# Performance work log

Measured on AMD Instinct MI355X. Metric: run time of the kernel, lower is better.

The kernel has to match this reference:

```python
import jax, jax.numpy as jnp
import numpy as np
from jax import lax

C = 256
B, T = 4, 4
AH, AW = 32, 32
VH, VW = 56, 56
EPS = 1e-5


def _pool_matrix(n_in, n_out):
    # PyTorch adaptive_avg_pool1d semantics per axis
    M = np.zeros((n_out, n_in), np.float32)
    for i in range(n_out):
        s = (i * n_in) // n_out
        e = -((-(i + 1) * n_in) // n_out)  # ceil
        M[i, s:e] = 1.0 / (e - s)
    return jnp.asarray(M)


def _bilinear_matrix(n_in, n_out):
    # PyTorch bilinear, align_corners=False
    scale = n_in / n_out
    M = np.zeros((n_out, n_in), np.float32)
    for i in range(n_out):
        src = (i + 0.5) * scale - 0.5
        src = min(max(src, 0.0), n_in - 1)
        i0 = int(np.floor(src))
        i1 = min(i0 + 1, n_in - 1)
        w1 = src - i0
        M[i, i0] += 1.0 - w1
        M[i, i1] += w1
    return jnp.asarray(M)


def _group_norm1(x, w, b):
    # GroupNorm(1, C): normalize over (C,H,W) per sample, per-channel affine
    mu = jnp.mean(x, axis=(1, 2, 3), keepdims=True)
    var = jnp.mean(jnp.square(x - mu), axis=(1, 2, 3), keepdims=True)
    xn = (x - mu) * lax.rsqrt(var + EPS)
    return xn * w[None, :, None, None] + b[None, :, None, None]


def _dwconv(x, w, pad, dil):
    c = x.shape[1]
    return lax.conv_general_dilated(
        x, w, window_strides=(1, 1), padding=[(pad, pad), (pad, pad)],
        rhs_dilation=(dil, dil), feature_group_count=c,
        dimension_numbers=('NCHW', 'OIHW', 'NCHW'))


def _pwconv(x, w, b):
    return jnp.einsum('oc,bchw->bohw', w, x) + b[None, :, None, None]


def _lkm(x, gn_w, gn_b, dw7, dw3, pw_w, pw_b):
    x = _group_norm1(x, gn_w, gn_b)
    x = _dwconv(x, dw7, pad=3, dil=1) + _dwconv(x, dw3, pad=3, dil=3)
    x = _pwconv(x, pw_w, pw_b)
    return jax.nn.gelu(x, approximate=False)


def setup_inputs() -> dict:
    key = jax.random.key(0)
    ks = jax.random.split(key, 20)
    s = lambda k, shape, scale=0.05: jax.random.normal(k, shape, jnp.float32) * scale
    return {
        'a': jax.random.normal(ks[0], (B, C, AH, AW), jnp.float32),
        'v': jax.random.normal(ks[1], (B * T, C, VH, VW), jnp.float32),
        'a_gn_w': jnp.ones((C,), jnp.float32), 'a_gn_b': jnp.zeros((C,), jnp.float32),
        'a_dw7': s(ks[2], (C, 1, 7, 7)), 'a_dw3': s(ks[3], (C, 1, 3, 3)),
        'a_pw_w': s(ks[4], (C, C)), 'a_pw_b': jnp.zeros((C,), jnp.float32),
        'v_gn_w': jnp.ones((C,), jnp.float32), 'v_gn_b': jnp.zeros((C,), jnp.float32),
        'v_dw7': s(ks[5], (C, 1, 7, 7)), 'v_dw3': s(ks[6], (C, 1, 3, 3)),
        'v_pw_w': s(ks[7], (C, C)), 'v_pw_b': jnp.zeros((C,), jnp.float32),
        'gate_a_w': s(ks[8], (C, C)), 'gate_a_b': jnp.zeros((C,), jnp.float32),
        'gate_v_w': s(ks[9], (C, C)), 'gate_v_b': jnp.zeros((C,), jnp.float32),
        'scale_a': jnp.ones((1,), jnp.float32), 'scale_v': jnp.ones((1,), jnp.float32),
    }


def reference(a, v, a_gn_w, a_gn_b, a_dw7, a_dw3, a_pw_w, a_pw_b,
              v_gn_w, v_gn_b, v_dw7, v_dw3, v_pw_w, v_pw_b,
              gate_a_w, gate_a_b, gate_v_w, gate_v_b, scale_a, scale_v):
    strength_a = strength_v = 1.0
    temp = 1.0
    b = a.shape[0]
    vb, c, vh, vw = v.shape
    t = vb // b
    ah, aw = a.shape[2], a.shape[3]

    a_feat = _lkm(a, a_gn_w, a_gn_b, a_dw7, a_dw3, a_pw_w, a_pw_b)
    v_feat = _lkm(v, v_gn_w, v_gn_b, v_dw7, v_dw3, v_pw_w, v_pw_b)

    v_feat_mean = v_feat.reshape(b, t, c, vh, vw).mean(axis=1) if t > 1 else v_feat

    if (vh, vw) != (ah, aw):
        Ph, Pw = _pool_matrix(vh, ah), _pool_matrix(vw, aw)
        v_for_a = jnp.einsum('oh,bchw,pw->bcop', Ph, v_feat_mean, Pw)
    else:
        v_for_a = v_feat_mean
    gate_a = jax.nn.sigmoid(_pwconv(v_for_a, gate_a_w, gate_a_b) / temp)

    if (ah, aw) != (vh, vw):
        Rh, Rw = _bilinear_matrix(ah, vh), _bilinear_matrix(aw, vw)
        a_for_v = jnp.einsum('oh,bchw,pw->bcop', Rh, a_feat, Rw)
    else:
        a_for_v = a_feat
    gate_v = jax.nn.sigmoid(_pwconv(a_for_v, gate_v_w, gate_v_b) / temp)
    if t > 1:
        gate_v = jnp.broadcast_to(gate_v[:, None], (b, t, c, vh, vw)).reshape(vb, c, vh, vw)

    a_out = a + strength_a * (scale_a[0] * (a_feat * gate_a))
    v_out = v + strength_v * (scale_v[0] * (v_feat * gate_v))
    return (a_out, v_out)
```

## Files before the change

kernel.cpp:

```cpp
#include <hip/hip_runtime.h>
#include <math.h>

#define C_   256
#define B_   4
#define T_   4
#define AH_  32
#define AW_  32
#define VH_  56
#define VW_  56
#define AHW  (AH_*AW_)
#define VHW  (VH_*VW_)
#define NA_  (B_*C_*AHW)
#define NV_  (B_*T_*C_*VHW)
#define NAV_ (B_*C_*VHW)

typedef unsigned short u16;
typedef short s16x8 __attribute__((ext_vector_type(8)));
typedef unsigned short u16x8 __attribute__((ext_vector_type(8)));
typedef unsigned short u16x4 __attribute__((ext_vector_type(4)));
typedef float f32x4 __attribute__((ext_vector_type(4)));

__device__ __forceinline__ u16 f2b(float f) {
  unsigned u = __float_as_uint(f);
  u += 0x7FFFu + ((u >> 16) & 1u);
  return (u16)(u >> 16);
}
__device__ __forceinline__ float b2f(u16 h) {
  return __uint_as_float((unsigned)h << 16);
}
__device__ __forceinline__ float gelu_f(float x) {
  float x2 = x * x;
  float e = __expf(x * (-1.5957691216f - 0.0713548162f * x2));
  return x * __builtin_amdgcn_rcpf(1.f + e);
}
__device__ __forceinline__ float sigmoid_f(float x) {
  return __builtin_amdgcn_rcpf(1.f + __expf(-x));
}

__global__ __launch_bounds__(256) void cvt_bf16_4(
    const float* __restrict__ s0, const float* __restrict__ s1,
    const float* __restrict__ s2, const float* __restrict__ s3,
    u16* __restrict__ dst)
{
  int g = blockIdx.x >> 5;
  const float* src = (g == 0) ? s0 : (g == 1) ? s1 : (g == 2) ? s2 : s3;
  size_t i = ((size_t)(blockIdx.x & 31) * 256 + threadIdx.x) * 8;
  float4 v0 = *(const float4*)(src + i);
  float4 v1 = *(const float4*)(src + i + 4);
  u16x8 o = {f2b(v0.x), f2b(v0.y), f2b(v0.z), f2b(v0.w),
             f2b(v1.x), f2b(v1.y), f2b(v1.z), f2b(v1.w)};
  *(u16x8*)(dst + (size_t)g * 65536 + i) = o;
}

__global__ __launch_bounds__(256) void gn_reduce1m(
    const float* __restrict__ a, const float* __restrict__ v,
    float* __restrict__ part)
{
  int samp = blockIdx.y, chunk = blockIdx.x;
  const float* x; int per;
  if (samp < 4) { x = a + (size_t)samp * (C_ * AHW); per = (C_ * AHW / 4) / 128; }
  else          { x = v + (size_t)(samp - 4) * (C_ * VHW); per = (C_ * VHW / 4) / 128; }
  const float4* xb = (const float4*)x + (size_t)chunk * per;
  float s = 0.f, s2 = 0.f;
  for (int i = threadIdx.x; i < per; i += 256) {
    float4 q = xb[i];
    s  += q.x + q.y + q.z + q.w;
    s2 += q.x*q.x + q.y*q.y + q.z*q.z + q.w*q.w;
  }
  __shared__ float sh1[256], sh2[256];
  sh1[threadIdx.x] = s; sh2[threadIdx.x] = s2;
  __syncthreads();
  for (int st = 128; st > 0; st >>= 1) {
    if (threadIdx.x < st) {
      sh1[threadIdx.x] += sh1[threadIdx.x + st];
      sh2[threadIdx.x] += sh2[threadIdx.x + st];
    }
    __syncthreads();
  }
  if (threadIdx.x == 0) {
    part[(samp * 128 + chunk) * 2 + 0] = sh1[0];
    part[(samp * 128 + chunk) * 2 + 1] = sh2[0];
  }
}

__global__ __launch_bounds__(128) void gn_reduce2m(
    const float* __restrict__ part, float* __restrict__ stats)
{
  int samp = blockIdx.x;
  int t = threadIdx.x;
  __shared__ float sh1[128], sh2[128];
  sh1[t] = part[(samp * 128 + t) * 2 + 0];
  sh2[t] = part[(samp * 128 + t) * 2 + 1];
  __syncthreads();
  for (int st = 64; st > 0; st >>= 1) {
    if (t < st) { sh1[t] += sh1[t + st]; sh2[t] += sh2[t + st]; }
    __syncthreads();
  }
  if (t == 0) {
    float invN = (samp < 4) ? 1.f / (float)(C_ * AHW) : 1.f / (float)(C_ * VHW);
    float mu  = sh1[0] * invN;
    float var = sh2[0] * invN - mu * mu;
    stats[samp * 2 + 0] = mu;
    stats[samp * 2 + 1] = rsqrtf(var + 1e-5f);
  }
}

__global__ __launch_bounds__(256) void gn_dwconv_all(
    const float* __restrict__ xa, const float* __restrict__ xv,
    const float* __restrict__ stats,
    const float* __restrict__ a_gn_w, const float* __restrict__ a_gn_b,
    const float* __restrict__ a_dw7, const float* __restrict__ a_dw3,
    const float* __restrict__ v_gn_w, const float* __restrict__ v_gn_b,
    const float* __restrict__ v_dw7, const float* __restrict__ v_dw3,
    u16* __restrict__ outa, u16* __restrict__ outv)
{
  __shared__ float tile[62 * 64];
  __shared__ float comb[49];
  const int t = threadIdx.x;
  if (blockIdx.x < 1024) {
    constexpr int TH = 38, TW = 38, TWP = 44;
    const int nc = blockIdx.x;
    const int n = nc >> 8, c = nc & 255;
    const float mu = stats[2 * n], rstd = stats[2 * n + 1];
    const float gsc = a_gn_w[c] * rstd;
    const float gsh = a_gn_b[c] - mu * gsc;
    if (t < 49) comb[t] = a_dw7[c * 49 + t];
    __syncthreads();
    if (t < 9) comb[(t / 3) * 21 + (t % 3) * 3] += a_dw3[c * 9 + t];
    const float* xc = xa + (size_t)nc * AHW;
    for (int idx = t; idx < TH * TW; idx += 256) {
      int th = idx / TW, tw = idx - th * TW;
      int h = th - 3, w = tw - 3;
      float val = 0.f;
      if (h >= 0 && h < 32 && w >= 0 && w < 32) val = xc[h * 32 + w] * gsc + gsh;
      tile[th * TWP + tw] = val;
    }
    __syncthreads();
    if (t < 128) {
      const int rg = t >> 3, cq = t & 7;
      const int r0 = rg * 2, w0 = cq * 4;
      float acc[2][4];
      #pragma unroll
      for (int r = 0; r < 2; ++r)
        #pragma unroll
        for (int j = 0; j < 4; ++j) acc[r][j] = 0.f;
      #pragma unroll
      for (int i = 0; i < 8; ++i) {
        const float* row = &tile[(r0 + i) * TWP + w0];
        float4 ra = *(const float4*)(row);
        float4 rb = *(const float4*)(row + 4);
        float2 rc = *(const float2*)(row + 8);
        float rr[10] = {ra.x, ra.y, ra.z, ra.w, rb.x, rb.y, rb.z, rb.w, rc.x, rc.y};
        #pragma unroll
        for (int ky = 0; ky < 7; ++ky) {
          int orow = i - ky;
          if (orow >= 0 && orow < 2) {
            #pragma unroll
            for (int kx = 0; kx < 7; ++kx) {
              float wg = comb[ky * 7 + kx];
              #pragma unroll
              for (int j = 0; j < 4; ++j)
                acc[orow][j] = fmaf(rr[kx + j], wg, acc[orow][j]);
            }
          }
        }
      }
      u16* oc = outa + (size_t)nc * AHW;
      #pragma unroll
      for (int r = 0; r < 2; ++r) {
        u16x4 res = {f2b(acc[r][0]), f2b(acc[r][1]), f2b(acc[r][2]), f2b(acc[r][3])};
        *(u16x4*)&oc[(r0 + r) * 32 + w0] = res;
      }
    }
  } else {
    const int nc = blockIdx.x - 1024;
    const int n = nc >> 8, c = nc & 255;
    const float mu = stats[8 + 2 * n], rstd = stats[8 + 2 * n + 1];
    const float gsc = v_gn_w[c] * rstd;
    const float gsh = v_gn_b[c] - mu * gsc;
    if (t < 49) comb[t] = v_dw7[c * 49 + t];
    __syncthreads();
    if (t < 9) comb[(t / 3) * 21 + (t % 3) * 3] += v_dw3[c * 9 + t];
    const float* xc = xv + (size_t)nc * VHW;
    if (t < 208) {
      int row, q;
      if (t < 96) { int ri = t >> 4; row = (ri < 3) ? ri : ri + 56; q = t & 15; }
      else        { int r = t - 96; row = 3 + (r >> 1); q = (r & 1) ? 15 : 0; }
      int qz = q ^ (row & 7);
      f32x4 z = {0.f, 0.f, 0.f, 0.f};
      *(f32x4*)&tile[row * 64 + qz * 4] = z;
    }
    #pragma unroll
    for (int it = 0; it < 4; ++it) {
      int idx = t + it * 256;
      if (idx < 784) {
        int row = idx / 14, q = idx - row * 14;
        float4 v = *(const float4*)(xc + row * VW_ + q * 4);
        int trow = row + 3;
        int tq = (q + 1) ^ (trow & 7);
        f32x4 sv = {v.x * gsc + gsh, v.y * gsc + gsh,
                    v.z * gsc + gsh, v.w * gsc + gsh};
        *(f32x4*)&tile[trow * 64 + tq * 4] = sv;
      }
    }
    __syncthreads();
    if (t < 196) {
      const int rg = t / 14, cq = t - rg * 14;
      const int r0 = rg * 4;
      float acc[4][4];
      #pragma unroll
      for (int r = 0; r < 4; ++r)
        #pragma unroll
        for (int j = 0; j < 4; ++j) acc[r][j] = 0.f;
      #pragma unroll
      for (int i = 0; i < 10; ++i) {
        int trow = r0 + i;
        const float* rowb = &tile[trow * 64];
        int rz = trow & 7;
        float rr[12];
        #pragma unroll
        for (int k = 0; k < 3; ++k) {
          int qk = (cq + k) ^ rz;
          f32x4 rv = *(const f32x4*)(rowb + qk * 4);
          rr[4 * k + 0] = rv[0]; rr[4 * k + 1] = rv[1];
          rr[4 * k + 2] = rv[2]; rr[4 * k + 3] = rv[3];
        }
        #pragma unroll
        for (int ky = 0; ky < 7; ++ky) {
          int orow = i - ky;
          if (orow >= 0 && orow < 4) {
            #pragma unroll
            for (int kx = 0; kx < 7; ++kx) {
              float wg = comb[ky * 7 + kx];
              #pragma unroll
              for (int j = 0; j < 4; ++j)
                acc[orow][j] = fmaf(rr[j + kx + 1], wg, acc[orow][j]);
            }
          }
        }
      }
      u16* oc = outv + (size_t)nc * VHW;
      #pragma unroll
      for (int r = 0; r < 4; ++r) {
        u16x4 res = {f2b(acc[r][0]), f2b(acc[r][1]), f2b(acc[r][2]), f2b(acc[r][3])};
        *(u16x4*)&oc[(r0 + r) * VW_ + cq * 4] = res;
      }
    }
  }
}

__global__ __launch_bounds__(256) void transpose_all(
    const u16* __restrict__ ina, u16* __restrict__ outa,
    const u16* __restrict__ inv, u16* __restrict__ outv)
{
  __shared__ u16 tile[64 * 68];
  const int t = threadIdx.x;
  int bid = blockIdx.x;
  const u16* in; u16* outp; int HW, PT;
  if (bid < 256) { in = ina; outp = outa; HW = AHW; PT = 16; }
  else           { bid -= 256; in = inv; outp = outv; HW = VHW; PT = 49; }
  int px = bid % PT; int rem = bid / PT;
  int cy = rem & 3, s = rem >> 2;
  const int p0 = px * 64, c0 = cy * 64;
  const u16* src = in + ((size_t)s * 256 + c0) * HW + p0;
  #pragma unroll
  for (int it = 0; it < 2; ++it) {
    int slot = it * 256 + t;
    int cr = slot >> 3, ch = slot & 7;
    u16x8 v = *(const u16x8*)(src + (size_t)cr * HW + ch * 8);
    u16x4 lo = {v[0], v[1], v[2], v[3]}, hi = {v[4], v[5], v[6], v[7]};
    *(u16x4*)&tile[cr * 68 + ch * 8] = lo;
    *(u16x4*)&tile[cr * 68 + ch * 8 + 4] = hi;
  }
  __syncthreads();
  int pr = t >> 2, ch = t & 3;
  u16* dst = outp + ((size_t)s * HW + p0 + pr) * 256 + c0;
  #pragma unroll
  for (int jj = 0; jj < 2; ++jj) {
    int cb = ch * 8 + jj * 32;
    u16x8 o;
    #pragma unroll
    for (int j = 0; j < 8; ++j) o[j] = tile[(cb + j) * 68 + pr];
    *(u16x8*)(dst + cb) = o;
  }
}

template<int ACT, int WPC, int WCP, int NBA, int PTA, int PTV>
__global__ __launch_bounds__(256) void mfma_pw2(
    const u16* __restrict__ Xa, const u16* __restrict__ Wa,
    const float* __restrict__ ba, u16* __restrict__ outa_pc, u16* __restrict__ outa_cp,
    const u16* __restrict__ Xv, const u16* __restrict__ Wv,
    const float* __restrict__ bv, u16* __restrict__ outv_pc, u16* __restrict__ outv_cp)
{
  __shared__ __align__(16) char smem[(256 * 72 + 64 * 72) * 2];
  u16* Wl = (u16*)smem;
  u16* Xl = (u16*)smem + 256 * 72;
  float* Tt = (float*)smem;
  u16*  Pc = (u16*)smem;
  const int t = threadIdx.x;
  const int lane = t & 63, wid = t >> 6;
  const int g = lane >> 4, lr = lane & 15;
  int bid = blockIdx.x;
  const u16 *X, *W; const float* bias; u16 *out_pc, *out_cp; int HW, px, s;
  if (bid < NBA) {
    X = Xa; W = Wa; bias = ba; out_pc = outa_pc; out_cp = outa_cp;
    HW = PTA * 64; px = bid % PTA; s = bid / PTA;
  } else {
    bid -= NBA;
    X = Xv; W = Wv; bias = bv; out_pc = outv_pc; out_cp = outv_cp;
    HW = PTV * 64; px = bid % PTV; s = bid / PTV;
  }
  const int p0 = px * 64;
  const u16* Xs = X + ((size_t)s * HW + p0) * 256;
  f32x4 acc[4][4] = {};
  u16x8 stw[8], stx[2];
  #pragma unroll
  for (int it = 0; it < 8; ++it) {
    int slot = it * 256 + t, row = slot >> 3, ch = slot & 7;
    stw[it] = *(const u16x8*)(W + row * 256 + ch * 8);
  }
  #pragma unroll
  for (int it = 0; it < 2; ++it) {
    int slot = it * 256 + t, row = slot >> 3, ch = slot & 7;
    stx[it] = *(const u16x8*)(Xs + (size_t)row * 256 + ch * 8);
  }
  for (int kt = 0; kt < 4; ++kt) {
    __syncthreads();
    #pragma unroll
    for (int it = 0; it < 8; ++it) {
      int slot = it * 256 + t, row = slot >> 3, ch = slot & 7;
      *(u16x8*)&Wl[row * 72 + ch * 8] = stw[it];
    }
    #pragma unroll
    for (int it = 0; it < 2; ++it) {
      int slot = it * 256 + t, row = slot >> 3, ch = slot & 7;
      *(u16x8*)&Xl[row * 72 + ch * 8] = stx[it];
    }
    __syncthreads();
    if (kt < 3) {
      const int k1 = (kt + 1) * 64;
      #pragma unroll
      for (int it = 0; it < 8; ++it) {
        int slot = it * 256 + t, row = slot >> 3, ch = slot & 7;
        stw[it] = *(const u16x8*)(W + row * 256 + k1 + ch * 8);
      }
      #pragma unroll
      for (int it = 0; it < 2; ++it) {
        int slot = it * 256 + t, row = slot >> 3, ch = slot & 7;
        stx[it] = *(const u16x8*)(Xs + (size_t)row * 256 + k1 + ch * 8);
      }
    }
    #pragma unroll
    for (int ks = 0; ks < 2; ++ks) {
      s16x8 af[4], bf[4];
      #pragma unroll
      for (int m = 0; m < 4; ++m) {
        int row = wid * 64 + m * 16 + lr;
        af[m] = *(const s16x8*)&Wl[row * 72 + ks * 32 + g * 8];
      }
      #pragma unroll
      for (int n = 0; n < 4; ++n) {
        int row = n * 16 + lr;
        bf[n] = *(const s16x8*)&Xl[row * 72 + ks * 32 + g * 8];
      }
      #pragma unroll
      for (int m = 0; m < 4; ++m)
        #pragma unroll
        for (int n = 0; n < 4; ++n)
          acc[m][n] = __builtin_amdgcn_mfma_f32_16x16x32_bf16(af[m], bf[n], acc[m][n], 0, 0, 0);
    }
  }
  __syncthreads();
  #pragma unroll
  for (int m = 0; m < 4; ++m) {
    int ob = wid * 64 + m * 16 + g * 4;
    float4 b4 = *(const float4*)&bias[ob];
    float bb[4] = {b4.x, b4.y, b4.z, b4.w};
    #pragma unroll
    for (int n = 0; n < 4; ++n)
      #pragma unroll
      for (int r = 0; r < 4; ++r) {
        float y = acc[m][n][r] + bb[r];
        acc[m][n][r] = (ACT == 0) ? gelu_f(y) : sigmoid_f(y);
      }
  }
  if (WPC) {
    #pragma unroll
    for (int m = 0; m < 4; ++m) {
      int obase = wid * 64 + m * 16 + g * 4;
      #pragma unroll
      for (int n = 0; n < 4; ++n) {
        int p = n * 16 + lr;
        int op = obase ^ ((p & 7) << 3);
        u16x4 pk = {f2b(acc[m][n][0]), f2b(acc[m][n][1]), f2b(acc[m][n][2]), f2b(acc[m][n][3])};
        *(u16x4*)&Pc[p * 256 + op] = pk;
      }
    }
    __syncthreads();
    int pr = t >> 2;
    u16* dst = out_pc + ((size_t)s * HW + p0 + pr) * 256;
    #pragma unroll
    for (int j = 0; j < 8; ++j) {
      int o = (j * 4 + (t & 3)) * 8;
      int op = o ^ ((pr & 7) << 3);
      u16x8 vv = *(const u16x8*)&Pc[pr * 256 + op];
      *(u16x8*)(dst + o) = vv;
    }
  }
  if (WCP) {
    #pragma unroll
    for (int ho = 0; ho < 2; ++ho) {
      __syncthreads();
      if ((wid >> 1) == ho) {
        #pragma unroll
        for (int m = 0; m < 4; ++m) {
          int ol = (wid & 1) * 64 + m * 16 + g * 4;
          #pragma unroll
          for (int n = 0; n < 4; ++n) {
            int p = n * 16 + lr, q = p >> 2;
            #pragma unroll
            for (int r = 0; r < 4; ++r) {
              int orow = ol + r;
              Tt[orow * 64 + ((q ^ (orow & 15)) << 2) + (p & 3)] = acc[m][n][r];
            }
          }
        }
      }
      __syncthreads();
      #pragma unroll
      for (int it = 0; it < 8; ++it) {
        int slot = it * 256 + t;
        int ol = slot >> 4, q = slot & 15;
        float4 v4 = *(const float4*)&Tt[ol * 64 + ((q ^ (ol & 15)) << 2)];
        u16x4 pk = {f2b(v4.x), f2b(v4.y), f2b(v4.z), f2b(v4.w)};
        int o = ho * 128 + ol;
        *(u16x4*)(out_cp + ((size_t)s * 256 + o) * HW + p0 + q * 4) = pk;
      }
    }
  }
}

__global__ __launch_bounds__(256) void pool_bilin(
    const u16* __restrict__ vf, u16* __restrict__ vfa,
    const u16* __restrict__ af, u16* __restrict__ afv)
{
  int c = threadIdx.x;
  int pb = blockIdx.x;
  if (pb < 4096) {
    int ow = pb & 31, oh = (pb >> 5) & 31, b = pb >> 10;
    int sh = (oh * VH_) >> 5, eh = ((oh + 1) * VH_ + 31) >> 5;
    int sw = (ow * VW_) >> 5, ew = ((ow + 1) * VW_ + 31) >> 5;
    float acc = 0.f;
    for (int tt = 0; tt < T_; ++tt)
      for (int ih = sh; ih < eh; ++ih)
        for (int iw = sw; iw < ew; ++iw)
          acc += b2f(vf[((size_t)(b * T_ + tt) * VHW + ih * VW_ + iw) * 256 + c]);
    vfa[(size_t)pb * 256 + c] = f2b(acc / (float)(T_ * (eh - sh) * (ew - sw)));
  } else {
    pb -= 4096;
    int ow = pb % VW_; int tmp = pb / VW_; int oh = tmp % VH_; int b = tmp / VH_;
    const float sc = (float)AH_ / (float)VH_;
    float srh = fminf(fmaxf((oh + 0.5f) * sc - 0.5f, 0.f), (float)(AH_ - 1));
    float srw = fminf(fmaxf((ow + 0.5f) * sc - 0.5f, 0.f), (float)(AW_ - 1));
    int h0 = (int)srh, w0 = (int)srw;
    int h1 = min(h0 + 1, AH_ - 1), w1 = min(w0 + 1, AW_ - 1);
    float fh = srh - (float)h0, fw = srw - (float)w0;
    const u16* base = af + (size_t)b * AHW * 256 + c;
    float v00 = b2f(base[(h0 * AW_ + w0) * 256]), v01 = b2f(base[(h0 * AW_ + w1) * 256]);
    float v10 = b2f(base[(h1 * AW_ + w0) * 256]), v11 = b2f(base[(h1 * AW_ + w1) * 256]);
    float top = v00 + (v01 - v00) * fw;
    float bot = v10 + (v11 - v10) * fw;
    afv[(size_t)pb * 256 + c] = f2b(top + (bot - top) * fh);
  }
}

__global__ __launch_bounds__(256) void final_av(
    const float* __restrict__ a, const u16* __restrict__ afcp,
    const u16* __restrict__ gacp, const float* __restrict__ sa,
    const float* __restrict__ v, const u16* __restrict__ vfcp,
    const u16* __restrict__ gvcp, const float* __restrict__ sv,
    float* __restrict__ out)
{
  int bid = blockIdx.x;
  if (bid < 512) {
    size_t i = ((size_t)bid * 256 + threadIdx.x) * 8;
    float s = sa[0];
    float4 a0 = *(const float4*)(a + i), a1 = *(const float4*)(a + i + 4);
    u16x8 f = *(const u16x8*)(afcp + i);
    u16x8 gg = *(const u16x8*)(gacp + i);
    float4 o0 = {a0.x + s * b2f(f[0]) * b2f(gg[0]), a0.y + s * b2f(f[1]) * b2f(gg[1]),
                 a0.z + s * b2f(f[2]) * b2f(gg[2]), a0.w + s * b2f(f[3]) * b2f(gg[3])};
    float4 o1 = {a1.x + s * b2f(f[4]) * b2f(gg[4]), a1.y + s * b2f(f[5]) * b2f(gg[5]),
                 a1.z + s * b2f(f[6]) * b2f(gg[6]), a1.w + s * b2f(f[7]) * b2f(gg[7])};
    *(float4*)(out + i) = o0;
    *(float4*)(out + i + 4) = o1;
  } else {
    size_t i = ((size_t)(bid - 512) * 256 + threadIdx.x) * 8;
    const size_t PER = (size_t)C_ * VHW;
    int bt = (int)(i / PER);
    size_t rem = i - (size_t)bt * PER;
    const u16* gp = gvcp + (size_t)(bt >> 2) * PER + rem;
    float s = sv[0];
    float4 v0 = *(const float4*)(v + i), v1 = *(const float4*)(v + i + 4);
    u16x8 f = *(const u16x8*)(vfcp + i);
    u16x8 gg = *(const u16x8*)gp;
    float4 o0 = {v0.x + s * b2f(f[0]) * b2f(gg[0]), v0.y + s * b2f(f[1]) * b2f(gg[1]),
                 v0.z + s * b2f(f[2]) * b2f(gg[2]), v0.w + s * b2f(f[3]) * b2f(gg[3])};
    float4 o1 = {v1.x + s * b2f(f[4]) * b2f(gg[4]), v1.y + s * b2f(f[5]) * b2f(gg[5]),
                 v1.z + s * b2f(f[6]) * b2f(gg[6]), v1.w + s * b2f(f[7]) * b2f(gg[7])};
    float* ov = out + NA_;
    *(float4*)(ov + i) = o0;
    *(float4*)(ov + i + 4) = o1;
  }
}

extern "C" void kernel_launch(void* const* d_in, const int* in_sizes, int n_in,
                              void* d_out, int out_size, void* d_ws, size_t ws_size,
                              hipStream_t stream)
{
  const float* a        = (const float*)d_in[0];
  const float* v        = (const float*)d_in[1];
  const float* a_gn_w   = (const float*)d_in[2];
  const float* a_gn_b   = (const float*)d_in[3];
  const float* a_dw7    = (const float*)d_in[4];
  const float* a_dw3    = (const float*)d_in[5];
  const float* a_pw_w   = (const float*)d_in[6];
  const float* a_pw_b   = (const float*)d_in[7];
  const float* v_gn_w   = (const float*)d_in[8];
  const float* v_gn_b   = (const float*)d_in[9];
  const float* v_dw7    = (const float*)d_in[10];
  const float* v_dw3    = (const float*)d_in[11];
  const float* v_pw_w   = (const float*)d_in[12];
  const float* v_pw_b   = (const float*)d_in[13];
  const float* gate_a_w = (const float*)d_in[14];
  const float* gate_a_b = (const float*)d_in[15];
  const float* gate_v_w = (const float*)d_in[16];
  const float* gate_v_b = (const float*)d_in[17];
  const float* scale_a  = (const float*)d_in[18];
  const float* scale_v  = (const float*)d_in[19];
  float* out = (float*)d_out;
  char* wsb = (char*)d_ws;

  const size_t SZ_V  = (size_t)NV_ * 2;
  const size_t SZ_AV = (size_t)NAV_ * 2;
  const size_t SZ_A  = (size_t)NA_ * 2;
  u16* dwv_b    = (u16*)(wsb + 0);
  u16* vfeat_cp = (u16*)(wsb + 0);
  u16* dwvT     = (u16*)(wsb + SZ_V);
  u16* afv      = (u16*)(wsb + SZ_V);
  u16* gatev_cp = (u16*)(wsb + SZ_V + SZ_AV);
  u16* vfeat_pc = (u16*)(wsb + 2 * SZ_V);
  u16* dwa_b    = (u16*)(wsb + 3 * SZ_V);
  u16* dwaT     = (u16*)(wsb + 3 * SZ_V + SZ_A);
  u16* afeat_pc = (u16*)(wsb + 3 * SZ_V + 2 * SZ_A);
  u16* afeat_cp = (u16*)(wsb + 3 * SZ_V + 3 * SZ_A);
  u16* vfa      = (u16*)(wsb + 3 * SZ_V + 4 * SZ_A);
  u16* gatea_cp = (u16*)(wsb + 3 * SZ_V + 5 * SZ_A);
  u16* w_bf     = (u16*)(wsb + 3 * SZ_V + 6 * SZ_A);
  float* pf     = (float*)(wsb + 3 * SZ_V + 6 * SZ_A + 4 * 65536 * 2);
  float* part   = pf;
  float* stats  = pf + 5120;
  u16* wA = w_bf, *wV = w_bf + 65536, *wGA = w_bf + 131072, *wGV = w_bf + 196608;

  cvt_bf16_4<<<128, 256, 0, stream>>>(a_pw_w, v_pw_w, gate_a_w, gate_v_w, w_bf);

  gn_reduce1m<<<dim3(128, 20), 256, 0, stream>>>(a, v, part);
  gn_reduce2m<<<20, 128, 0, stream>>>(part, stats);

  gn_dwconv_all<<<5120, 256, 0, stream>>>(a, v, stats,
      a_gn_w, a_gn_b, a_dw7, a_dw3, v_gn_w, v_gn_b, v_dw7, v_dw3, dwa_b, dwv_b);

  transpose_all<<<3392, 256, 0, stream>>>(dwa_b, dwaT, dwv_b, dwvT);

  mfma_pw2<0, 1, 1, 64, 16, 49><<<848, 256, 0, stream>>>(
      dwaT, wA, a_pw_b, afeat_pc, afeat_cp,
      dwvT, wV, v_pw_b, vfeat_pc, vfeat_cp);

  pool_bilin<<<16640, 256, 0, stream>>>(vfeat_pc, vfa, afeat_pc, afv);

  mfma_pw2<1, 0, 1, 64, 16, 49><<<260, 256, 0, stream>>>(
      vfa, wGA, gate_a_b, nullptr, gatea_cp,
      afv, wGV, gate_v_b, nullptr, gatev_cp);

  final_av<<<6784, 256, 0, stream>>>(a, afeat_cp, gatea_cp, scale_a,
                                     v, vfeat_cp, gatev_cp, scale_v, out);
}
```

Before: 148.0 us.

## Read channel-major activations directly in pointwise GEMM, drop transpose and pc outputs

The pointwise MFMA kernel now loads channel-major (NCHW) activations and transposes them into LDS itself, so the separate transpose kernel is gone. It also stops writing the pixel-major copy of the features, and pool/bilinear is rewritten to work on channel-major data, one block per (batch, channel). This removes a full read and write of the large v intermediates plus one launch. In exchange the GEMM's global loads become narrower strided 8-byte reads, and the pooling access pattern changes.

```diff
diff --git a/kernel.cpp b/kernel.cpp
--- a/kernel.cpp
+++ b/kernel.cpp
@@ -249,81 +249,44 @@
   }
 }
 
-__global__ __launch_bounds__(256) void transpose_all(
-    const u16* __restrict__ ina, u16* __restrict__ outa,
-    const u16* __restrict__ inv, u16* __restrict__ outv)
-{
-  __shared__ u16 tile[64 * 68];
-  const int t = threadIdx.x;
-  int bid = blockIdx.x;
-  const u16* in; u16* outp; int HW, PT;
-  if (bid < 256) { in = ina; outp = outa; HW = AHW; PT = 16; }
-  else           { bid -= 256; in = inv; outp = outv; HW = VHW; PT = 49; }
-  int px = bid % PT; int rem = bid / PT;
-  int cy = rem & 3, s = rem >> 2;
-  const int p0 = px * 64, c0 = cy * 64;
-  const u16* src = in + ((size_t)s * 256 + c0) * HW + p0;
-  #pragma unroll
-  for (int it = 0; it < 2; ++it) {
-    int slot = it * 256 + t;
-    int cr = slot >> 3, ch = slot & 7;
-    u16x8 v = *(const u16x8*)(src + (size_t)cr * HW + ch * 8);
-    u16x4 lo = {v[0], v[1], v[2], v[3]}, hi = {v[4], v[5], v[6], v[7]};
-    *(u16x4*)&tile[cr * 68 + ch * 8] = lo;
-    *(u16x4*)&tile[cr * 68 + ch * 8 + 4] = hi;
-  }
-  __syncthreads();
-  int pr = t >> 2, ch = t & 3;
-  u16* dst = outp + ((size_t)s * HW + p0 + pr) * 256 + c0;
-  #pragma unroll
-  for (int jj = 0; jj < 2; ++jj) {
-    int cb = ch * 8 + jj * 32;
-    u16x8 o;
-    #pragma unroll
-    for (int j = 0; j < 8; ++j) o[j] = tile[(cb + j) * 68 + pr];
-    *(u16x8*)(dst + cb) = o;
-  }
-}
-
-template<int ACT, int WPC, int WCP, int NBA, int PTA, int PTV>
+template<int ACT, int NBA, int PTA, int PTV>
 __global__ __launch_bounds__(256) void mfma_pw2(
     const u16* __restrict__ Xa, const u16* __restrict__ Wa,
-    const float* __restrict__ ba, u16* __restrict__ outa_pc, u16* __restrict__ outa_cp,
+    const float* __restrict__ ba, u16* __restrict__ outa_cp,
     const u16* __restrict__ Xv, const u16* __restrict__ Wv,
-    const float* __restrict__ bv, u16* __restrict__ outv_pc, u16* __restrict__ outv_cp)
-{
-  __shared__ __align__(16) char smem[(256 * 72 + 64 * 72) * 2];
+    const float* __restrict__ bv, u16* __restrict__ outv_cp)
+{
+  __shared__ __align__(16) char smem[256 * 72 * 2 + 64 * 68 * 2];
   u16* Wl = (u16*)smem;
   u16* Xl = (u16*)smem + 256 * 72;
   float* Tt = (float*)smem;
-  u16*  Pc = (u16*)smem;
   const int t = threadIdx.x;
   const int lane = t & 63, wid = t >> 6;
   const int g = lane >> 4, lr = lane & 15;
   int bid = blockIdx.x;
-  const u16 *X, *W; const float* bias; u16 *out_pc, *out_cp; int HW, px, s;
+  const u16 *X, *W; const float* bias; u16* out_cp; int HW, px, s;
   if (bid < NBA) {
-    X = Xa; W = Wa; bias = ba; out_pc = outa_pc; out_cp = outa_cp;
+    X = Xa; W = Wa; bias = ba; out_cp = outa_cp;
     HW = PTA * 64; px = bid % PTA; s = bid / PTA;
   } else {
     bid -= NBA;
-    X = Xv; W = Wv; bias = bv; out_pc = outv_pc; out_cp = outv_cp;
+    X = Xv; W = Wv; bias = bv; out_cp = outv_cp;
     HW = PTV * 64; px = bid % PTV; s = bid / PTV;
   }
   const int p0 = px * 64;
-  const u16* Xs = X + ((size_t)s * HW + p0) * 256;
+  const u16* Xs = X + (size_t)s * 256 * HW + p0;
+  const int cg = t >> 4, pg = t & 15;
   f32x4 acc[4][4] = {};
-  u16x8 stw[8], stx[2];
+  u16x8 stw[8];
+  u16x4 stc[4];
   #pragma unroll
   for (int it = 0; it < 8; ++it) {
     int slot = it * 256 + t, row = slot >> 3, ch = slot & 7;
     stw[it] = *(const u16x8*)(W + row * 256 + ch * 8);
   }
   #pragma unroll
-  for (int it = 0; it < 2; ++it) {
-    int slot = it * 256 + t, row = slot >> 3, ch = slot & 7;
-    stx[it] = *(const u16x8*)(Xs + (size_t)row * 256 + ch * 8);
-  }
+  for (int cc = 0; cc < 4; ++cc)
+    stc[cc] = *(const u16x4*)(Xs + (size_t)(cg * 4 + cc) * HW + pg * 4);
   for (int kt = 0; kt < 4; ++kt) {
     __syncthreads();
     #pragma unroll
@@ -332,9 +295,9 @@
       *(u16x8*)&Wl[row * 72 + ch * 8] = stw[it];
     }
     #pragma unroll
-    for (int it = 0; it < 2; ++it) {
-      int slot = it * 256 + t, row = slot >> 3, ch = slot & 7;
-      *(u16x8*)&Xl[row * 72 + ch * 8] = stx[it];
+    for (int pp = 0; pp < 4; ++pp) {
+      u16x4 vv = {stc[0][pp], stc[1][pp], stc[2][pp], stc[3][pp]};
+      *(u16x4*)&Xl[(pg * 4 + pp) * 68 + cg * 4] = vv;
     }
     __syncthreads();
     if (kt < 3) {
@@ -345,10 +308,8 @@
         stw[it] = *(const u16x8*)(W + row * 256 + k1 + ch * 8);
       }
       #pragma unroll
-      for (int it = 0; it < 2; ++it) {
-        int slot = it * 256 + t, row = slot >> 3, ch = slot & 7;
-        stx[it] = *(const u16x8*)(Xs + (size_t)row * 256 + k1 + ch * 8);
-      }
+      for (int cc = 0; cc < 4; ++cc)
+        stc[cc] = *(const u16x4*)(Xs + (size_t)(k1 + cg * 4 + cc) * HW + pg * 4);
     }
     #pragma unroll
     for (int ks = 0; ks < 2; ++ks) {
@@ -361,7 +322,7 @@
       #pragma unroll
       for (int n = 0; n < 4; ++n) {
         int row = n * 16 + lr;
-        bf[n] = *(const s16x8*)&Xl[row * 72 + ks * 32 + g * 8];
+        bf[n] = *(const s16x8*)&Xl[row * 68 + ks * 32 + g * 8];
       }
       #pragma unroll
       for (int m = 0; m < 4; ++m)
@@ -384,93 +345,83 @@
         acc[m][n][r] = (ACT == 0) ? gelu_f(y) : sigmoid_f(y);
       }
   }
-  if (WPC) {
-    #pragma unroll
-    for (int m = 0; m < 4; ++m) {
-      int obase = wid * 64 + m * 16 + g * 4;
-      #pragma unroll
-      for (int n = 0; n < 4; ++n) {
-        int p = n * 16 + lr;
-        int op = obase ^ ((p & 7) << 3);
-        u16x4 pk = {f2b(acc[m][n][0]), f2b(acc[m][n][1]), f2b(acc[m][n][2]), f2b(acc[m][n][3])};
-        *(u16x4*)&Pc[p * 256 + op] = pk;
-      }
-    }
-    __syncthreads();
-    int pr = t >> 2;
-    u16* dst = out_pc + ((size_t)s * HW + p0 + pr) * 256;
-    #pragma unroll
-    for (int j = 0; j < 8; ++j) {
-      int o = (j * 4 + (t & 3)) * 8;
-      int op = o ^ ((pr & 7) << 3);
-      u16x8 vv = *(const u16x8*)&Pc[pr * 256 + op];
-      *(u16x8*)(dst + o) = vv;
-    }
-  }
-  if (WCP) {
-    #pragma unroll
-    for (int ho = 0; ho < 2; ++ho) {
-      __syncthreads();
-      if ((wid >> 1) == ho) {
-        #pragma unroll
-        for (int m = 0; m < 4; ++m) {
-          int ol = (wid & 1) * 64 + m * 16 + g * 4;
+  #pragma unroll
+  for (int ho = 0; ho < 2; ++ho) {
+    __syncthreads();
+    if ((wid >> 1) == ho) {
+      #pragma unroll
+      for (int m = 0; m < 4; ++m) {
+        int ol = (wid & 1) * 64 + m * 16 + g * 4;
+        #pragma unroll
+        for (int n = 0; n < 4; ++n) {
+          int p = n * 16 + lr, q = p >> 2;
           #pragma unroll
-          for (int n = 0; n < 4; ++n) {
-            int p = n * 16 + lr, q = p >> 2;
-            #pragma unroll
-            for (int r = 0; r < 4; ++r) {
-              int orow = ol + r;
-              Tt[orow * 64 + ((q ^ (orow & 15)) << 2) + (p & 3)] = acc[m][n][r];
-            }
+          for (int r = 0; r < 4; ++r) {
+            int orow = ol + r;
+            Tt[orow * 64 + ((q ^ (orow & 15)) << 2) + (p & 3)] = acc[m][n][r];
           }
         }
       }
-      __syncthreads();
-      #pragma unroll
-      for (int it = 0; it < 8; ++it) {
-        int slot = it * 256 + t;
-        int ol = slot >> 4, q = slot & 15;
-        float4 v4 = *(const float4*)&Tt[ol * 64 + ((q ^ (ol & 15)) << 2)];
-        u16x4 pk = {f2b(v4.x), f2b(v4.y), f2b(v4.z), f2b(v4.w)};
-        int o = ho * 128 + ol;
-        *(u16x4*)(out_cp + ((size_t)s * 256 + o) * HW + p0 + q * 4) = pk;
-      }
-    }
-  }
-}
-
-__global__ __launch_bounds__(256) void pool_bilin(
-    const u16* __restrict__ vf, u16* __restrict__ vfa,
-    const u16* __restrict__ af, u16* __restrict__ afv)
-{
-  int c = threadIdx.x;
-  int pb = blockIdx.x;
-  if (pb < 4096) {
-    int ow = pb & 31, oh = (pb >> 5) & 31, b = pb >> 10;
-    int sh = (oh * VH_) >> 5, eh = ((oh + 1) * VH_ + 31) >> 5;
-    int sw = (ow * VW_) >> 5, ew = ((ow + 1) * VW_ + 31) >> 5;
-    float acc = 0.f;
-    for (int tt = 0; tt < T_; ++tt)
-      for (int ih = sh; ih < eh; ++ih)
-        for (int iw = sw; iw < ew; ++iw)
-          acc += b2f(vf[((size_t)(b * T_ + tt) * VHW + ih * VW_ + iw) * 256 + c]);
-    vfa[(size_t)pb * 256 + c] = f2b(acc / (float)(T_ * (eh - sh) * (ew - sw)));
+    }
+    __syncthreads();
+    #pragma unroll
+    for (int it = 0; it < 8; ++it) {
+      int slot = it * 256 + t;
+      int ol = slot >> 4, q = slot & 15;
+      float4 v4 = *(const float4*)&Tt[ol * 64 + ((q ^ (ol & 15)) << 2)];
+      u16x4 pk = {f2b(v4.x), f2b(v4.y), f2b(v4.z), f2b(v4.w)};
+      int o = ho * 128 + ol;
+      *(u16x4*)(out_cp + ((size_t)s * 256 + o) * HW + p0 + q * 4) = pk;
+    }
+  }
+}
+
+__global__ __launch_bounds__(256) void pool_bilin_cp(
+    const u16* __restrict__ vf_cp, u16* __restrict__ vfa_cp,
+    const u16* __restrict__ af_cp, u16* __restrict__ afv_cp)
+{
+  const int t = threadIdx.x;
+  int bid = blockIdx.x;
+  if (bid < 1024) {
+    int b = bid >> 8, c = bid & 255;
+    u16* dst = vfa_cp + ((size_t)(b * 256 + c) << 10);
+    #pragma unroll
+    for (int k = 0; k < 4; ++k) {
+      int idx = t + k * 256;
+      int oh = idx >> 5, ow = idx & 31;
+      int sh = (oh * VH_) >> 5, eh = ((oh + 1) * VH_ + 31) >> 5;
+      int sw = (ow * VW_) >> 5, ew = ((ow + 1) * VW_ + 31) >> 5;
+      float acc = 0.f;
+      for (int tt = 0; tt < T_; ++tt) {
+        const u16* base = vf_cp + ((size_t)((b * T_ + tt) * 256 + c)) * VHW;
+        for (int ih = sh; ih < eh; ++ih)
+          for (int iw = sw; iw < ew; ++iw)
+            acc += b2f(base[ih * VW_ + iw]);
+      }
+      dst[idx] = f2b(acc / (float)(T_ * (eh - sh) * (ew - sw)));
+    }
   } else {
-    pb -= 4096;
-    int ow = pb % VW_; int tmp = pb / VW_; int oh = tmp % VH_; int b = tmp / VH_;
+    bid -= 1024;
+    int b = bid >> 8, c = bid & 255;
+    const u16* base = af_cp + ((size_t)(b * 256 + c) << 10);
+    u16* dst = afv_cp + (size_t)(b * 256 + c) * VHW;
     const float sc = (float)AH_ / (float)VH_;
-    float srh = fminf(fmaxf((oh + 0.5f) * sc - 0.5f, 0.f), (float)(AH_ - 1));
-    float srw = fminf(fmaxf((ow + 0.5f) * sc - 0.5f, 0.f), (float)(AW_ - 1));
-    int h0 = (int)srh, w0 = (int)srw;
-    int h1 = min(h0 + 1, AH_ - 1), w1 = min(w0 + 1, AW_ - 1);
-    float fh = srh - (float)h0, fw = srw - (float)w0;
-    const u16* base = af + (size_t)b * AHW * 256 + c;
-    float v00 = b2f(base[(h0 * AW_ + w0) * 256]), v01 = b2f(base[(h0 * AW_ + w1) * 256]);
-    float v10 = b2f(base[(h1 * AW_ + w0) * 256]), v11 = b2f(base[(h1 * AW_ + w1) * 256]);
-    float top = v00 + (v01 - v00) * fw;
-    float bot = v10 + (v11 - v10) * fw;
-    afv[(size_t)pb * 256 + c] = f2b(top + (bot - top) * fh);
+    for (int k = 0; k < 13; ++k) {
+      int idx = t + k * 256;
+      if (idx < VHW) {
+        int oh = idx / VW_, ow = idx - oh * VW_;
+        float srh = fminf(fmaxf((oh + 0.5f) * sc - 0.5f, 0.f), (float)(AH_ - 1));
+        float srw = fminf(fmaxf((ow + 0.5f) * sc - 0.5f, 0.f), (float)(AW_ - 1));
+        int h0 = (int)srh, w0 = (int)srw;
+        int h1 = min(h0 + 1, AH_ - 1), w1 = min(w0 + 1, AW_ - 1);
+        float fh = srh - (float)h0, fw = srw - (float)w0;
+        float v00 = b2f(base[h0 * AW_ + w0]), v01 = b2f(base[h0 * AW_ + w1]);
+        float v10 = b2f(base[h1 * AW_ + w0]), v11 = b2f(base[h1 * AW_ + w1]);
+        float top = v00 + (v01 - v00) * fw;
+        float bot = v10 + (v11 - v10) * fw;
+        dst[idx] = f2b(top + (bot - top) * fh);
+      }
+    }
   }
 }
 
@@ -545,19 +496,15 @@
   const size_t SZ_AV = (size_t)NAV_ * 2;
   const size_t SZ_A  = (size_t)NA_ * 2;
   u16* dwv_b    = (u16*)(wsb + 0);
-  u16* vfeat_cp = (u16*)(wsb + 0);
-  u16* dwvT     = (u16*)(wsb + SZ_V);
-  u16* afv      = (u16*)(wsb + SZ_V);
-  u16* gatev_cp = (u16*)(wsb + SZ_V + SZ_AV);
-  u16* vfeat_pc = (u16*)(wsb + 2 * SZ_V);
-  u16* dwa_b    = (u16*)(wsb + 3 * SZ_V);
-  u16* dwaT     = (u16*)(wsb + 3 * SZ_V + SZ_A);
-  u16* afeat_pc = (u16*)(wsb + 3 * SZ_V + 2 * SZ_A);
-  u16* afeat_cp = (u16*)(wsb + 3 * SZ_V + 3 * SZ_A);
-  u16* vfa      = (u16*)(wsb + 3 * SZ_V + 4 * SZ_A);
-  u16* gatea_cp = (u16*)(wsb + 3 * SZ_V + 5 * SZ_A);
-  u16* w_bf     = (u16*)(wsb + 3 * SZ_V + 6 * SZ_A);
-  float* pf     = (float*)(wsb + 3 * SZ_V + 6 * SZ_A + 4 * 65536 * 2);
+  u16* afv      = (u16*)(wsb + 0);
+  u16* gatev_cp = (u16*)(wsb + SZ_AV);
+  u16* vfeat_cp = (u16*)(wsb + SZ_V);
+  u16* dwa_b    = (u16*)(wsb + 2 * SZ_V);
+  u16* afeat_cp = (u16*)(wsb + 2 * SZ_V + SZ_A);
+  u16* vfa      = (u16*)(wsb + 2 * SZ_V + 2 * SZ_A);
+  u16* gatea_cp = (u16*)(wsb + 2 * SZ_V + 3 * SZ_A);
+  u16* w_bf     = (u16*)(wsb + 2 * SZ_V + 4 * SZ_A);
+  float* pf     = (float*)(wsb + 2 * SZ_V + 4 * SZ_A + 4 * 65536 * 2);
   float* part   = pf;
   float* stats  = pf + 5120;
   u16* wA = w_bf, *wV = w_bf + 65536, *wGA = w_bf + 131072, *wGV = w_bf + 196608;
@@ -570,17 +517,15 @@
   gn_dwconv_all<<<5120, 256, 0, stream>>>(a, v, stats,
       a_gn_w, a_gn_b, a_dw7, a_dw3, v_gn_w, v_gn_b, v_dw7, v_dw3, dwa_b, dwv_b);
 
-  transpose_all<<<3392, 256, 0, stream>>>(dwa_b, dwaT, dwv_b, dwvT);
-
-  mfma_pw2<0, 1, 1, 64, 16, 49><<<848, 256, 0, stream>>>(
-      dwaT, wA, a_pw_b, afeat_pc, afeat_cp,
-      dwvT, wV, v_pw_b, vfeat_pc, vfeat_cp);
-
-  pool_bilin<<<16640, 256, 0, stream>>>(vfeat_pc, vfa, afeat_pc, afv);
-
-  mfma_pw2<1, 0, 1, 64, 16, 49><<<260, 256, 0, stream>>>(
-      vfa, wGA, gate_a_b, nullptr, gatea_cp,
-      afv, wGV, gate_v_b, nullptr, gatev_cp);
+  mfma_pw2<0, 64, 16, 49><<<848, 256, 0, stream>>>(
+      dwa_b, wA, a_pw_b, afeat_cp,
+      dwv_b, wV, v_pw_b, vfeat_cp);
+
+  pool_bilin_cp<<<2048, 256, 0, stream>>>(vfeat_cp, vfa, afeat_cp, afv);
+
+  mfma_pw2<1, 64, 16, 49><<<260, 256, 0, stream>>>(
+      vfa, wGA, gate_a_b, gatea_cp,
+      afv, wGV, gate_v_b, gatev_cp);
 
   final_av<<<6784, 256, 0, stream>>>(a, afeat_cp, gatea_cp, scale_a,
                                      v, vfeat_cp, gatev_cp, scale_v, out);
```

Result: slower. 159.7 us (+7.9%).
